# Performance work log

Hardware: AMD Instinct MI355X
Metric: run time of the kernel (lower is better)

The kernel has to match this reference:

```python
import jax, jax.numpy as jnp
import numpy as np

PI = 3.14159265358979323846
MARGIN = 6.0
DIM = 256
ENT_TOT = 43234
REL_RANGE = (6.0 + 2.0) / DIM  # (margin + epsilon) / dim = 0.03125


def setup_inputs() -> dict:
    key = jax.random.key(0)
    k1, k2, k3 = jax.random.split(key, 3)
    head = jax.random.normal(k1, (32, 2 * DIM), dtype=jnp.float32)
    relation = jax.random.normal(k2, (32, DIM), dtype=jnp.float32)
    ent_emb = jax.random.normal(k3, (ENT_TOT, 2 * DIM), dtype=jnp.float32)
    return {"head": head, "relation": relation, "ent_emb": ent_emb}


def reference(head, relation, ent_emb):
    # head: (B, 2D) -> re/im halves (B, D)
    re_h, im_h = jnp.split(head, 2, axis=-1)
    # entity table: (E, 2D) -> (E, D) each
    re_t, im_t = jnp.split(ent_emb, 2, axis=-1)
    # phase rotation from relation embedding
    phase = relation / (REL_RANGE / PI)          # (B, D)
    re_r = jnp.cos(phase)
    im_r = jnp.sin(phase)
    # complex rotation of head by relation: (B, D)
    re_rot = re_h * re_r - im_h * im_r
    im_rot = re_h * im_r + im_h * re_r
    # difference against every entity, broadcast to (B, E, D)
    re_s = re_rot[:, None, :] - re_t[None, :, :]
    im_s = im_rot[:, None, :] - im_t[None, :, :]
    # L2 norm over the complex pair, summed over D -> (B, E)
    dist = jnp.sqrt(re_s * re_s + im_s * im_s).sum(axis=-1)
    return MARGIN - dist
```

## Files before the change

kernel.cpp:

```cpp
#include <hip/hip_runtime.h>
#include <math.h>

#define DIMH 256
#define NB   32
#define E_TOT 43234
#define TE   64
#define DK   32
#define NC   (DIMH / DK)
#define PHASE_DIV 0.009947183943243459f

typedef float v2f __attribute__((ext_vector_type(2)));

__device__ __forceinline__ unsigned bf16_rne(float f) {
    unsigned u = __float_as_uint(f);
    return (u + 0x7FFFu + ((u >> 16) & 1u)) >> 16;
}
__device__ __forceinline__ unsigned pack_bf16(float f0, float f1) {
    return bf16_rne(f0) | (bf16_rne(f1) << 16);
}
__device__ __forceinline__ v2f unpack_bf16(unsigned w) {
    v2f r;
    r.x = __uint_as_float(w << 16);
    r.y = __uint_as_float(w & 0xFFFF0000u);
    return r;
}

__global__ __launch_bounds__(256) void rot_kernel(const float* __restrict__ head,
                                                  const float* __restrict__ rel,
                                                  uint2* __restrict__ rot_bf) {
    int i  = blockIdx.x * 256 + threadIdx.x;
    int b  = i >> 7;
    int dp = i & 127;
    int d0 = dp * 2;
    float re0, re1, im0, im1;
    {
        float re_h = head[b * 2 * DIMH + d0];
        float im_h = head[b * 2 * DIMH + DIMH + d0];
        float s, c;
        sincosf(rel[b * DIMH + d0] / PHASE_DIV, &s, &c);
        re0 = re_h * c - im_h * s;
        im0 = re_h * s + im_h * c;
    }
    {
        float re_h = head[b * 2 * DIMH + d0 + 1];
        float im_h = head[b * 2 * DIMH + DIMH + d0 + 1];
        float s, c;
        sincosf(rel[b * DIMH + d0 + 1] / PHASE_DIV, &s, &c);
        re1 = re_h * c - im_h * s;
        im1 = re_h * s + im_h * c;
    }
    uint2 w;
    w.x = pack_bf16(re0, re1);
    w.y = pack_bf16(im0, im1);
    rot_bf[b * (DIMH / 2) + dp] = w;
}

__device__ __forceinline__ v2f sqrt2(v2f s) {
    v2f r;
    r.x = __builtin_amdgcn_sqrtf(s.x);
    r.y = __builtin_amdgcn_sqrtf(s.y);
    return r;
}

__global__ __launch_bounds__(256, 4) void dist_kernel(const float* __restrict__ ent,
                                                      const uint2* __restrict__ rot_bf,
                                                      float* __restrict__ out) {
    __shared__ uint2 s_e[TE][DK / 2 + 1];
    __shared__ uint2 s_r[NB][DK / 2 + 1];

    const int tid = threadIdx.x;
    const int eb  = blockIdx.x * TE;
    const int eg  = tid & 31;
    const int bg  = (tid >> 5) * 4;

    const int row0 = tid >> 3;
    const int row1 = (tid + 256) >> 3;
    const int c4   = tid & 7;
    const int er0  = min(eb + row0, E_TOT - 1);
    const int er1  = min(eb + row1, E_TOT - 1);
    const int rrow0 = tid >> 4;
    const int rrow1 = (tid + 256) >> 4;
    const int rpp   = tid & 15;

    float4 pre[2], pim[2];
    uint2  prt[2];

    auto load_chunk = [&](int c) {
        const int dk = c * DK;
        const float* b0 = &ent[(size_t)er0 * (2 * DIMH)];
        const float* b1 = &ent[(size_t)er1 * (2 * DIMH)];
        pre[0] = *reinterpret_cast<const float4*>(b0 + dk + 4 * c4);
        pim[0] = *reinterpret_cast<const float4*>(b0 + DIMH + dk + 4 * c4);
        pre[1] = *reinterpret_cast<const float4*>(b1 + dk + 4 * c4);
        pim[1] = *reinterpret_cast<const float4*>(b1 + DIMH + dk + 4 * c4);
        prt[0] = rot_bf[rrow0 * (DIMH / 2) + c * (DK / 2) + rpp];
        prt[1] = rot_bf[rrow1 * (DIMH / 2) + c * (DK / 2) + rpp];
    };

    v2f acc[4][2];
    #pragma unroll
    for (int j = 0; j < 4; ++j)
        #pragma unroll
        for (int k = 0; k < 2; ++k) { acc[j][k].x = 0.f; acc[j][k].y = 0.f; }

    load_chunk(0);

    for (int c = 0; c < NC; ++c) {
        {
            const int rows[2] = {row0, row1};
            #pragma unroll
            for (int it = 0; it < 2; ++it) {
                uint2 w0, w1;
                w0.x = pack_bf16(pre[it].x, pre[it].y);
                w0.y = pack_bf16(pim[it].x, pim[it].y);
                w1.x = pack_bf16(pre[it].z, pre[it].w);
                w1.y = pack_bf16(pim[it].z, pim[it].w);
                s_e[rows[it]][2 * c4]     = w0;
                s_e[rows[it]][2 * c4 + 1] = w1;
            }
            s_r[rrow0][rpp] = prt[0];
            s_r[rrow1][rpp] = prt[1];
        }
        __syncthreads();

        if (c + 1 < NC) load_chunk(c + 1);

        #pragma unroll 4
        for (int p = 0; p < DK / 2; ++p) {
            v2f rr[4], ri[4], er[2], ei[2];
            #pragma unroll
            for (int j = 0; j < 4; ++j) {
                uint2 w = s_r[bg + j][p];
                rr[j] = unpack_bf16(w.x);
                ri[j] = unpack_bf16(w.y);
            }
            #pragma unroll
            for (int k = 0; k < 2; ++k) {
                uint2 w = s_e[eg + 32 * k][p];
                er[k] = unpack_bf16(w.x);
                ei[k] = unpack_bf16(w.y);
            }
            #pragma unroll
            for (int j = 0; j < 4; ++j)
                #pragma unroll
                for (int k = 0; k < 2; ++k) {
                    v2f a = rr[j] - er[k];
                    v2f b = ri[j] - ei[k];
                    v2f s = a * a + b * b;
                    acc[j][k] += sqrt2(s);
                }
        }
        __syncthreads();
    }

    #pragma unroll
    for (int k = 0; k < 2; ++k) {
        int e = eb + eg + 32 * k;
        if (e < E_TOT) {
            #pragma unroll
            for (int j = 0; j < 4; ++j)
                out[(size_t)(bg + j) * E_TOT + e] = 6.0f - (acc[j][k].x + acc[j][k].y);
        }
    }
}

extern "C" void kernel_launch(void* const* d_in, const int* in_sizes, int n_in,
                              void* d_out, int out_size, void* d_ws, size_t ws_size,
                              hipStream_t stream) {
    const float* head = (const float*)d_in[0];
    const float* rel  = (const float*)d_in[1];
    const float* ent  = (const float*)d_in[2];
    uint2* rot_bf = (uint2*)d_ws;

    rot_kernel<<<(NB * DIMH / 2) / 256, 256, 0, stream>>>(head, rel, rot_bf);

    int etiles = (E_TOT + TE - 1) / TE;
    dist_kernel<<<etiles, 256, 0, stream>>>(ent, rot_bf, (float*)d_out);
}
```

Measured before the change: 184.3 us.

## Store staged operands in fp32 and shrink entity tile to 32 rows

Measured after the change: 174.8 us. -5.2%, faster.

```diff
diff --git a/kernel.cpp b/kernel.cpp
--- a/kernel.cpp
+++ b/kernel.cpp
@@ -4,55 +4,39 @@
 #define DIMH 256
 #define NB   32
 #define E_TOT 43234
-#define TE   64
+#define TE   32
 #define DK   32
 #define NC   (DIMH / DK)
 #define PHASE_DIV 0.009947183943243459f
 
 typedef float v2f __attribute__((ext_vector_type(2)));
-
-__device__ __forceinline__ unsigned bf16_rne(float f) {
-    unsigned u = __float_as_uint(f);
-    return (u + 0x7FFFu + ((u >> 16) & 1u)) >> 16;
-}
-__device__ __forceinline__ unsigned pack_bf16(float f0, float f1) {
-    return bf16_rne(f0) | (bf16_rne(f1) << 16);
-}
-__device__ __forceinline__ v2f unpack_bf16(unsigned w) {
-    v2f r;
-    r.x = __uint_as_float(w << 16);
-    r.y = __uint_as_float(w & 0xFFFF0000u);
-    return r;
-}
+typedef float v4f __attribute__((ext_vector_type(4)));
 
 __global__ __launch_bounds__(256) void rot_kernel(const float* __restrict__ head,
                                                   const float* __restrict__ rel,
-                                                  uint2* __restrict__ rot_bf) {
+                                                  float4* __restrict__ rot_v4) {
     int i  = blockIdx.x * 256 + threadIdx.x;
     int b  = i >> 7;
     int dp = i & 127;
     int d0 = dp * 2;
-    float re0, re1, im0, im1;
+    float4 w;
     {
         float re_h = head[b * 2 * DIMH + d0];
         float im_h = head[b * 2 * DIMH + DIMH + d0];
         float s, c;
         sincosf(rel[b * DIMH + d0] / PHASE_DIV, &s, &c);
-        re0 = re_h * c - im_h * s;
-        im0 = re_h * s + im_h * c;
+        w.x = re_h * c - im_h * s;
+        w.z = re_h * s + im_h * c;
     }
     {
         float re_h = head[b * 2 * DIMH + d0 + 1];
         float im_h = head[b * 2 * DIMH + DIMH + d0 + 1];
         float s, c;
         sincosf(rel[b * DIMH + d0 + 1] / PHASE_DIV, &s, &c);
-        re1 = re_h * c - im_h * s;
-        im1 = re_h * s + im_h * c;
+        w.y = re_h * c - im_h * s;
+        w.w = re_h * s + im_h * c;
     }
-    uint2 w;
-    w.x = pack_bf16(re0, re1);
-    w.y = pack_bf16(im0, im1);
-    rot_bf[b * (DIMH / 2) + dp] = w;
+    rot_v4[b * (DIMH / 2) + dp] = w;
 }
 
 __device__ __forceinline__ v2f sqrt2(v2f s) {
@@ -62,44 +46,37 @@
     return r;
 }
 
-__global__ __launch_bounds__(256, 4) void dist_kernel(const float* __restrict__ ent,
-                                                      const uint2* __restrict__ rot_bf,
+__global__ __launch_bounds__(256, 6) void dist_kernel(const float* __restrict__ ent,
+                                                      const float4* __restrict__ rot_v4,
                                                       float* __restrict__ out) {
-    __shared__ uint2 s_e[TE][DK / 2 + 1];
-    __shared__ uint2 s_r[NB][DK / 2 + 1];
+    __shared__ v4f s_e[TE][DK / 2 + 1];
+    __shared__ v4f s_r[NB][DK / 2 + 1];
 
     const int tid = threadIdx.x;
     const int eb  = blockIdx.x * TE;
-    const int eg  = tid & 31;
-    const int bg  = (tid >> 5) * 4;
+    const int ep  = tid & 15;
+    const int bp  = tid >> 4;
 
-    const int row0 = tid >> 3;
-    const int row1 = (tid + 256) >> 3;
+    const int srow = tid >> 3;
     const int c4   = tid & 7;
-    const int er0  = min(eb + row0, E_TOT - 1);
-    const int er1  = min(eb + row1, E_TOT - 1);
-    const int rrow0 = tid >> 4;
-    const int rrow1 = (tid + 256) >> 4;
-    const int rpp   = tid & 15;
+    const int er   = min(eb + srow, E_TOT - 1);
+    const int rrow = tid >> 4;
+    const int rdp  = tid & 15;
 
-    float4 pre[2], pim[2];
-    uint2  prt[2];
+    float4 p_re, p_im, p_r0, p_r1;
 
     auto load_chunk = [&](int c) {
         const int dk = c * DK;
-        const float* b0 = &ent[(size_t)er0 * (2 * DIMH)];
-        const float* b1 = &ent[(size_t)er1 * (2 * DIMH)];
-        pre[0] = *reinterpret_cast<const float4*>(b0 + dk + 4 * c4);
-        pim[0] = *reinterpret_cast<const float4*>(b0 + DIMH + dk + 4 * c4);
-        pre[1] = *reinterpret_cast<const float4*>(b1 + dk + 4 * c4);
-        pim[1] = *reinterpret_cast<const float4*>(b1 + DIMH + dk + 4 * c4);
-        prt[0] = rot_bf[rrow0 * (DIMH / 2) + c * (DK / 2) + rpp];
-        prt[1] = rot_bf[rrow1 * (DIMH / 2) + c * (DK / 2) + rpp];
+        const float* b0 = &ent[(size_t)er * (2 * DIMH)];
+        p_re = *reinterpret_cast<const float4*>(b0 + dk + 4 * c4);
+        p_im = *reinterpret_cast<const float4*>(b0 + DIMH + dk + 4 * c4);
+        p_r0 = rot_v4[rrow * (DIMH / 2) + c * (DK / 2) + rdp];
+        p_r1 = rot_v4[(rrow + 16) * (DIMH / 2) + c * (DK / 2) + rdp];
     };
 
-    v2f acc[4][2];
+    v2f acc[2][2];
     #pragma unroll
-    for (int j = 0; j < 4; ++j)
+    for (int j = 0; j < 2; ++j)
         #pragma unroll
         for (int k = 0; k < 2; ++k) { acc[j][k].x = 0.f; acc[j][k].y = 0.f; }
 
@@ -107,19 +84,16 @@
 
     for (int c = 0; c < NC; ++c) {
         {
-            const int rows[2] = {row0, row1};
-            #pragma unroll
-            for (int it = 0; it < 2; ++it) {
-                uint2 w0, w1;
-                w0.x = pack_bf16(pre[it].x, pre[it].y);
-                w0.y = pack_bf16(pim[it].x, pim[it].y);
-                w1.x = pack_bf16(pre[it].z, pre[it].w);
-                w1.y = pack_bf16(pim[it].z, pim[it].w);
-                s_e[rows[it]][2 * c4]     = w0;
-                s_e[rows[it]][2 * c4 + 1] = w1;
-            }
-            s_r[rrow0][rpp] = prt[0];
-            s_r[rrow1][rpp] = prt[1];
+            v4f lo, hi;
+            lo.x = p_re.x; lo.y = p_re.y; lo.z = p_im.x; lo.w = p_im.y;
+            hi.x = p_re.z; hi.y = p_re.w; hi.z = p_im.z; hi.w = p_im.w;
+            s_e[srow][2 * c4]     = lo;
+            s_e[srow][2 * c4 + 1] = hi;
+            v4f r0, r1;
+            r0.x = p_r0.x; r0.y = p_r0.y; r0.z = p_r0.z; r0.w = p_r0.w;
+            r1.x = p_r1.x; r1.y = p_r1.y; r1.z = p_r1.z; r1.w = p_r1.w;
+            s_r[rrow][rdp]      = r0;
+            s_r[rrow + 16][rdp] = r1;
         }
         __syncthreads();
 
@@ -127,39 +101,30 @@
 
         #pragma unroll 4
         for (int p = 0; p < DK / 2; ++p) {
-            v2f rr[4], ri[4], er[2], ei[2];
-            #pragma unroll
-            for (int j = 0; j < 4; ++j) {
-                uint2 w = s_r[bg + j][p];
-                rr[j] = unpack_bf16(w.x);
-                ri[j] = unpack_bf16(w.y);
-            }
-            #pragma unroll
-            for (int k = 0; k < 2; ++k) {
-                uint2 w = s_e[eg + 32 * k][p];
-                er[k] = unpack_bf16(w.x);
-                ei[k] = unpack_bf16(w.y);
-            }
-            #pragma unroll
-            for (int j = 0; j < 4; ++j)
-                #pragma unroll
-                for (int k = 0; k < 2; ++k) {
-                    v2f a = rr[j] - er[k];
-                    v2f b = ri[j] - ei[k];
-                    v2f s = a * a + b * b;
-                    acc[j][k] += sqrt2(s);
-                }
+            v4f r0 = s_r[2 * bp][p];
+            v4f r1 = s_r[2 * bp + 1][p];
+            v4f e0 = s_e[ep][p];
+            v4f e1 = s_e[ep + 16][p];
+
+            {   v2f a = r0.xy - e0.xy, b = r0.zw - e0.zw;
+                acc[0][0] += sqrt2(a * a + b * b); }
+            {   v2f a = r0.xy - e1.xy, b = r0.zw - e1.zw;
+                acc[0][1] += sqrt2(a * a + b * b); }
+            {   v2f a = r1.xy - e0.xy, b = r1.zw - e0.zw;
+                acc[1][0] += sqrt2(a * a + b * b); }
+            {   v2f a = r1.xy - e1.xy, b = r1.zw - e1.zw;
+                acc[1][1] += sqrt2(a * a + b * b); }
         }
         __syncthreads();
     }
 
     #pragma unroll
     for (int k = 0; k < 2; ++k) {
-        int e = eb + eg + 32 * k;
+        int e = eb + ep + 16 * k;
         if (e < E_TOT) {
             #pragma unroll
-            for (int j = 0; j < 4; ++j)
-                out[(size_t)(bg + j) * E_TOT + e] = 6.0f - (acc[j][k].x + acc[j][k].y);
+            for (int j = 0; j < 2; ++j)
+                out[(size_t)(2 * bp + j) * E_TOT + e] = 6.0f - (acc[j][k].x + acc[j][k].y);
         }
     }
 }
@@ -170,10 +135,10 @@
     const float* head = (const float*)d_in[0];
     const float* rel  = (const float*)d_in[1];
     const float* ent  = (const float*)d_in[2];
-    uint2* rot_bf = (uint2*)d_ws;
+    float4* rot_v4 = (float4*)d_ws;
 
-    rot_kernel<<<(NB * DIMH / 2) / 256, 256, 0, stream>>>(head, rel, rot_bf);
+    rot_kernel<<<(NB * DIMH / 2) / 256, 256, 0, stream>>>(head, rel, rot_v4);
 
     int etiles = (E_TOT + TE - 1) / TE;
-    dist_kernel<<<etiles, 256, 0, stream>>>(ent, rot_bf, (float*)d_out);
+    dist_kernel<<<etiles, 256, 0, stream>>>(ent, rot_v4, (float*)d_out);
 }
```
